# Optimization experiments

Hardware: AMD Instinct MI355X
Metric: run time of the kernel (lower is better)

## Reference

```python
import jax, jax.numpy as jnp
import numpy as np

VOCAB, EMB, HID, FF, NCLS = 1000, 32, 32, 16, 7
T, B = 512, 512


def setup_inputs() -> dict:
    key = jax.random.key(0)
    ks = jax.random.split(key, 10)
    s = 1.0 / np.sqrt(HID)
    return {
        "x": jax.random.randint(ks[0], (T, B), 0, VOCAB, dtype=jnp.int64)
        if jax.config.jax_enable_x64 else jax.random.randint(ks[0], (T, B), 0, VOCAB, dtype=jnp.int32),
        "emb": jax.random.normal(ks[1], (VOCAB, EMB), dtype=jnp.float32),
        "W_ih": jax.random.uniform(ks[2], (4 * HID, EMB), minval=-s, maxval=s, dtype=jnp.float32),
        "W_hh": jax.random.uniform(ks[3], (4 * HID, HID), minval=-s, maxval=s, dtype=jnp.float32),
        "b_ih": jax.random.uniform(ks[4], (4 * HID,), minval=-s, maxval=s, dtype=jnp.float32),
        "b_hh": jax.random.uniform(ks[5], (4 * HID,), minval=-s, maxval=s, dtype=jnp.float32),
        "W1": jax.random.uniform(ks[6], (FF, HID), minval=-s, maxval=s, dtype=jnp.float32),
        "b1": jax.random.uniform(ks[7], (FF,), minval=-s, maxval=s, dtype=jnp.float32),
        "W2": jax.random.uniform(ks[8], (NCLS, FF), minval=-s, maxval=s, dtype=jnp.float32),
        "b2": jax.random.uniform(ks[9], (NCLS,), minval=-s, maxval=s, dtype=jnp.float32),
    }


def _lstm(xg, W_hh):
    # xg: (T, B, 4H) precomputed input-to-gate projections (incl. both biases)
    Bn = xg.shape[1]
    h0 = jnp.zeros((Bn, HID), xg.dtype)
    c0 = jnp.zeros((Bn, HID), xg.dtype)

    def step(carry, xg_t):
        h, c = carry
        g = xg_t + h @ W_hh.T  # (B, 4H)
        i, f, gg, o = jnp.split(g, 4, axis=-1)  # PyTorch gate order i,f,g,o
        i = jax.nn.sigmoid(i)
        f = jax.nn.sigmoid(f)
        gg = jnp.tanh(gg)
        o = jax.nn.sigmoid(o)
        c = f * c + i * gg
        h = o * jnp.tanh(c)
        return (h, c), h

    _, hs = jax.lax.scan(step, (h0, c0), xg)
    return hs  # (T, B, H)


def reference(x, emb, W_ih, W_hh, b_ih, b_hh, W1, b1, W2, b2):
    e = emb[x]  # (T, B, EMB) embedding lookup
    xg = jnp.einsum('tbe,ge->tbg', e, W_ih) + b_ih + b_hh  # (T, B, 4H)
    hs = _lstm(xg, W_hh)  # (T, B, H)
    z = jax.nn.relu(jnp.einsum('tbh,fh->tbf', hs, W1) + b1)  # (T, B, FF)
    logits = jnp.einsum('tbf,cf->tbc', z, W2) + b2  # (T, B, NCLS)
    # torch F.softmax with dim=None on a 3D tensor softmaxes over dim 0
    return jax.nn.softmax(logits, axis=0)
```

## Files before the change

### kernel.cpp

```cpp
#include <hip/hip_runtime.h>
#include <math.h>

#define TT    512
#define BB    512
#define HID   32
#define EMB   32
#define FFD   16
#define NCLS  7
#define VOCABN 1000

typedef float v2f __attribute__((ext_vector_type(2)));
typedef float v4f __attribute__((ext_vector_type(4)));

#define NLOG2E  (-1.4426950408889634f)
#define N2LOG2E (-2.8853900817779268f)

__device__ __forceinline__ float rl(float v, int k) {
    return __int_as_float(__builtin_amdgcn_readlane(__float_as_int(v), k));
}
__device__ __forceinline__ float fast_rcp(float x) {
#if defined(__has_builtin)
#if __has_builtin(__builtin_amdgcn_rcpf)
    return __builtin_amdgcn_rcpf(x);
#else
    return 1.0f / x;
#endif
#else
    return 1.0f / x;
#endif
}
__device__ __forceinline__ float sigf(float x) { return fast_rcp(1.0f + __expf(-x)); }
__device__ __forceinline__ float tanh_fast(float x) { return 2.0f * sigf(2.0f * x) - 1.0f; }

__device__ __forceinline__ v2f fma2(v2f a, v2f b, v2f c) {
#if defined(__has_builtin)
#if __has_builtin(__builtin_elementwise_fma)
    return __builtin_elementwise_fma(a, b, c);
#else
    v2f r; r.x = fmaf(a.x, b.x, c.x); r.y = fmaf(a.y, b.y, c.y); return r;
#endif
#else
    v2f r; r.x = fmaf(a.x, b.x, c.x); r.y = fmaf(a.y, b.y, c.y); return r;
#endif
}

__device__ __forceinline__ float xhalf_swap(float v) {
#if defined(__has_builtin)
#if __has_builtin(__builtin_amdgcn_permlane32_swap)
    const unsigned u = __float_as_uint(v);
    auto r = __builtin_amdgcn_permlane32_swap(u, u, false, false);
    return __uint_as_float((r[0] ^ r[1]) ^ u);
#else
    return __shfl_xor(v, 32);
#endif
#else
    return __shfl_xor(v, 32);
#endif
}

__global__ __launch_bounds__(64) void build_xg(
    const float* __restrict__ emb, const float* __restrict__ W_ih,
    const float* __restrict__ b_ih, const float* __restrict__ b_hh,
    float2* __restrict__ tab, int scaled)
{
    const int v = blockIdx.x;
    const int j = threadIdx.x;
    const float* e  = emb + v * EMB;
    const float* w0 = W_ih + j * EMB;
    const float* w1 = W_ih + (j + 64) * EMB;
    float a0 = b_ih[j]      + b_hh[j];
    float a1 = b_ih[j + 64] + b_hh[j + 64];
    #pragma unroll
    for (int k = 0; k < EMB; ++k) {
        const float ek = e[k];
        a0 = fmaf(w0[k], ek, a0);
        a1 = fmaf(w1[k], ek, a1);
    }
    float s0 = 1.0f, s1 = 1.0f;
    if (scaled) { s0 = NLOG2E; s1 = (j < 32) ? N2LOG2E : NLOG2E; }
    tab[v * 64 + j] = make_float2(a0 * s0, a1 * s1);
}

__global__ __launch_bounds__(64)
__attribute__((amdgpu_waves_per_eu(1, 1)))
void lstm_fused(
    const int* __restrict__ x, const float2* __restrict__ tab,
    const float* __restrict__ W_hh,
    const float* __restrict__ W1, const float* __restrict__ b1,
    const float* __restrict__ W2, const float* __restrict__ b2,
    float* __restrict__ out)
{
    const int b  = blockIdx.x;
    const int j  = threadIdx.x;
    const int m  = j & 31;
    const bool lo = j < 32;

    __shared__ __align__(16) float sh[8 * HID];
    __shared__ __align__(16) float shlg2[TT][17];

    const float fA = NLOG2E;
    const float fB = lo ? N2LOG2E : NLOG2E;
    const v2f sA2 = {fA, fA};
    const v2f sB2 = {fB, fB};
    const v4f* WA = (const v4f*)(W_hh + j * HID);
    const v4f* WB = (const v4f*)(W_hh + (j + 64) * HID);
    v4f t;
    v2f wpa0,wpa1,wpa2,wpa3,wpa4,wpa5,wpa6,wpa7,wpa8,wpa9,wpa10,wpa11,wpa12,wpa13,wpa14,wpa15;
    v2f wpb0,wpb1,wpb2,wpb3,wpb4,wpb5,wpb6,wpb7,wpb8,wpb9,wpb10,wpb11,wpb12,wpb13,wpb14,wpb15;
    t = WA[0]; wpa0  = t.lo * sA2; wpa1  = t.hi * sA2;
    t = WA[1]; wpa2  = t.lo * sA2; wpa3  = t.hi * sA2;
    t = WA[2]; wpa4  = t.lo * sA2; wpa5  = t.hi * sA2;
    t = WA[3]; wpa6  = t.lo * sA2; wpa7  = t.hi * sA2;
    t = WA[4]; wpa8  = t.lo * sA2; wpa9  = t.hi * sA2;
    t = WA[5]; wpa10 = t.lo * sA2; wpa11 = t.hi * sA2;
    t = WA[6]; wpa12 = t.lo * sA2; wpa13 = t.hi * sA2;
    t = WA[7]; wpa14 = t.lo * sA2; wpa15 = t.hi * sA2;
    t = WB[0]; wpb0  = t.lo * sB2; wpb1  = t.hi * sB2;
    t = WB[1]; wpb2  = t.lo * sB2; wpb3  = t.hi * sB2;
    t = WB[2]; wpb4  = t.lo * sB2; wpb5  = t.hi * sB2;
    t = WB[3]; wpb6  = t.lo * sB2; wpb7  = t.hi * sB2;
    t = WB[4]; wpb8  = t.lo * sB2; wpb9  = t.hi * sB2;
    t = WB[5]; wpb10 = t.lo * sB2; wpb11 = t.hi * sB2;
    t = WB[6]; wpb12 = t.lo * sB2; wpb13 = t.hi * sB2;
    t = WB[7]; wpb14 = t.lo * sB2; wpb15 = t.hi * sB2;

    const int f16 = j & 15;
    v2f w1p0,w1p1,w1p2,w1p3,w1p4,w1p5,w1p6,w1p7,w1p8,w1p9,w1p10,w1p11,w1p12,w1p13,w1p14,w1p15;
    {
        const v4f* W1r = (const v4f*)(W1 + f16 * HID);
        v4f q;
        q = W1r[0]; w1p0  = q.lo; w1p1  = q.hi;
        q = W1r[1]; w1p2  = q.lo; w1p3  = q.hi;
        q = W1r[2]; w1p4  = q.lo; w1p5  = q.hi;
        q = W1r[3]; w1p6  = q.lo; w1p7  = q.hi;
        q = W1r[4]; w1p8  = q.lo; w1p9  = q.hi;
        q = W1r[5]; w1p10 = q.lo; w1p11 = q.hi;
        q = W1r[6]; w1p12 = q.lo; w1p13 = q.hi;
        q = W1r[7]; w1p14 = q.lo; w1p15 = q.hi;
    }
    const float b1v = b1[f16];

    float h = 0.f, c = 0.f;

    auto z_store = [&](int t_out, v4f h0, v4f h1, v4f h2, v4f h3,
                                  v4f h4, v4f h5, v4f h6, v4f h7) {
        v2f z0 = {b1v, 0.f}, z1 = {0.f, 0.f};
        z0 = fma2(w1p0,  h0.lo, z0);  z1 = fma2(w1p1,  h0.hi, z1);
        z0 = fma2(w1p2,  h1.lo, z0);  z1 = fma2(w1p3,  h1.hi, z1);
        z0 = fma2(w1p4,  h2.lo, z0);  z1 = fma2(w1p5,  h2.hi, z1);
        z0 = fma2(w1p6,  h3.lo, z0);  z1 = fma2(w1p7,  h3.hi, z1);
        z0 = fma2(w1p8,  h4.lo, z0);  z1 = fma2(w1p9,  h4.hi, z1);
        z0 = fma2(w1p10, h5.lo, z0);  z1 = fma2(w1p11, h5.hi, z1);
        z0 = fma2(w1p12, h6.lo, z0);  z1 = fma2(w1p13, h6.hi, z1);
        z0 = fma2(w1p14, h7.lo, z0);  z1 = fma2(w1p15, h7.hi, z1);
        const v2f zs = z0 + z1;
        const float z = fmaxf(zs.x + zs.y, 0.0f);
        if (j < 16) shlg2[t_out][j] = z;
    };

    if (lo) sh[7 * HID + m] = 0.0f;

    int xiB[8];
    float2 cxg[8];
    {
        int xi0[8];
        #pragma unroll
        for (int u = 0; u < 8; ++u) xi0[u] = x[u * BB + b];
        #pragma unroll
        for (int u = 0; u < 8; ++u) xiB[u] = x[(8 + u) * BB + b];
        #pragma unroll
        for (int u = 0; u < 8; ++u) cxg[u] = tab[(size_t)xi0[u] * 64 + j];
    }

    for (int t8 = 0; t8 < TT / 8; ++t8) {
        float2 nxg[8];
        #pragma unroll
        for (int u = 0; u < 8; ++u) nxg[u] = tab[(size_t)xiB[u] * 64 + j];
        int xiN[8];
        const int nb2 = (t8 + 2 < TT / 8) ? (t8 + 2) * 8 : 0;
        #pragma unroll
        for (int u = 0; u < 8; ++u) xiN[u] = x[(nb2 + u) * BB + b];

        #pragma unroll
        for (int u = 0; u < 8; ++u) {
            const float* hb = sh + ((u + 7) & 7) * HID;
            const v4f h0 = *(const v4f*)(hb + 0);
            const v4f h1 = *(const v4f*)(hb + 4);
            const v4f h2 = *(const v4f*)(hb + 8);
            const v4f h3 = *(const v4f*)(hb + 12);
            const v4f h4 = *(const v4f*)(hb + 16);
            const v4f h5 = *(const v4f*)(hb + 20);
            const v4f h6 = *(const v4f*)(hb + 24);
            const v4f h7 = *(const v4f*)(hb + 28);

            v2f aP0 = {cxg[u].x, 0.f}, aP1 = {0.f, 0.f};
            v2f aQ0 = {cxg[u].y, 0.f}, aQ1 = {0.f, 0.f};
            aP0 = fma2(wpa0,  h0.lo, aP0);  aP1 = fma2(wpa1,  h0.hi, aP1);
            aQ0 = fma2(wpb0,  h0.lo, aQ0);  aQ1 = fma2(wpb1,  h0.hi, aQ1);
            aP0 = fma2(wpa2,  h1.lo, aP0);  aP1 = fma2(wpa3,  h1.hi, aP1);
            aQ0 = fma2(wpb2,  h1.lo, aQ0);  aQ1 = fma2(wpb3,  h1.hi, aQ1);
            aP0 = fma2(wpa4,  h2.lo, aP0);  aP1 = fma2(wpa5,  h2.hi, aP1);
            aQ0 = fma2(wpb4,  h2.lo, aQ0);  aQ1 = fma2(wpb5,  h2.hi, aQ1);
            aP0 = fma2(wpa6,  h3.lo, aP0);  aP1 = fma2(wpa7,  h3.hi, aP1);
            aQ0 = fma2(wpb6,  h3.lo, aQ0);  aQ1 = fma2(wpb7,  h3.hi, aQ1);
            aP0 = fma2(wpa8,  h4.lo, aP0);  aP1 = fma2(wpa9,  h4.hi, aP1);
            aQ0 = fma2(wpb8,  h4.lo, aQ0);  aQ1 = fma2(wpb9,  h4.hi, aQ1);
            aP0 = fma2(wpa10, h5.lo, aP0);  aP1 = fma2(wpa11, h5.hi, aP1);
            aQ0 = fma2(wpb10, h5.lo, aQ0);  aQ1 = fma2(wpb11, h5.hi, aQ1);
            aP0 = fma2(wpa12, h6.lo, aP0);  aP1 = fma2(wpa13, h6.hi, aP1);
            aQ0 = fma2(wpb12, h6.lo, aQ0);  aQ1 = fma2(wpb13, h6.hi, aQ1);
            aP0 = fma2(wpa14, h7.lo, aP0);  aP1 = fma2(wpa15, h7.hi, aP1);
            aQ0 = fma2(wpb14, h7.lo, aQ0);  aQ1 = fma2(wpb15, h7.hi, aQ1);
            const v2f aP = aP0 + aP1;
            const v2f aQ = aQ0 + aQ1;
            const float accA = aP.x + aP.y;
            const float accB = aQ.x + aQ.y;

            const float actA = fast_rcp(1.0f + __builtin_exp2f(accA));
            const float sgB  = fast_rcp(1.0f + __builtin_exp2f(accB));
            const float actB = lo ? fmaf(2.0f, sgB, -1.0f) : sgB;
            const float oA = xhalf_swap(actA);
            const float oB = xhalf_swap(actB);
            const float gi = lo ? actA : oA;
            const float gf = lo ? oA   : actA;
            const float gg = lo ? actB : oB;
            const float go = lo ? oB   : actB;
            c = fmaf(gf, c, gi * gg);
            const float tc = fmaf(2.0f,
                fast_rcp(1.0f + __builtin_exp2f(c * N2LOG2E)), -1.0f);
            h = go * tc;

            if (lo) sh[u * HID + m] = h;

            if (t8 + u > 0)
                z_store(t8 * 8 + u - 1, h0, h1, h2, h3, h4, h5, h6, h7);
        }

        #pragma unroll
        for (int u = 0; u < 8; ++u) { cxg[u] = nxg[u]; xiB[u] = xiN[u]; }
    }

    {
        const float* hb = sh + 7 * HID;
        const v4f h0 = *(const v4f*)(hb + 0);
        const v4f h1 = *(const v4f*)(hb + 4);
        const v4f h2 = *(const v4f*)(hb + 8);
        const v4f h3 = *(const v4f*)(hb + 12);
        const v4f h4 = *(const v4f*)(hb + 16);
        const v4f h5 = *(const v4f*)(hb + 20);
        const v4f h6 = *(const v4f*)(hb + 24);
        const v4f h7 = *(const v4f*)(hb + 28);
        z_store(TT - 1, h0, h1, h2, h3, h4, h5, h6, h7);
    }

    float lg[8][NCLS];
    #pragma unroll
    for (int i = 0; i < 8; ++i) {
        const int tt = j + 64 * i;
        float zz[FFD];
        #pragma unroll
        for (int f = 0; f < FFD; ++f) zz[f] = shlg2[tt][f];
        #pragma unroll
        for (int cc = 0; cc < NCLS; ++cc) {
            float a0 = b2[cc], a1 = 0.f, a2 = 0.f, a3 = 0.f;
            #pragma unroll
            for (int f = 0; f < FFD; f += 4) {
                a0 = fmaf(W2[cc * FFD + f],     zz[f],     a0);
                a1 = fmaf(W2[cc * FFD + f + 1], zz[f + 1], a1);
                a2 = fmaf(W2[cc * FFD + f + 2], zz[f + 2], a2);
                a3 = fmaf(W2[cc * FFD + f + 3], zz[f + 3], a3);
            }
            lg[i][cc] = (a0 + a1) + (a2 + a3);
        }
    }
    #pragma unroll
    for (int cc = 0; cc < NCLS; ++cc) {
        float mm = lg[0][cc];
        #pragma unroll
        for (int i = 1; i < 8; ++i) mm = fmaxf(mm, lg[i][cc]);
        #pragma unroll
        for (int off = 32; off; off >>= 1) mm = fmaxf(mm, __shfl_xor(mm, off));
        float ss = 0.f;
        #pragma unroll
        for (int i = 0; i < 8; ++i) { lg[i][cc] = __expf(lg[i][cc] - mm); ss += lg[i][cc]; }
        #pragma unroll
        for (int off = 32; off; off >>= 1) ss += __shfl_xor(ss, off);
        const float ic = fast_rcp(ss);
        #pragma unroll
        for (int i = 0; i < 8; ++i) lg[i][cc] *= ic;
    }
    #pragma unroll
    for (int i = 0; i < 8; ++i) {
        const int tt = j + 64 * i;
        float* op = out + ((size_t)tt * BB + b) * NCLS;
        #pragma unroll
        for (int cc = 0; cc < NCLS; ++cc) op[cc] = lg[i][cc];
    }
}

template <bool TAB>
__global__ __launch_bounds__(64) void lstm_all(
    const int* __restrict__ x, const float* __restrict__ emb,
    const float* __restrict__ W_ih, const float* __restrict__ W_hh,
    const float* __restrict__ b_ih, const float* __restrict__ b_hh,
    const float* __restrict__ W1, const float* __restrict__ b1,
    const float* __restrict__ W2, const float* __restrict__ b2,
    const float2* __restrict__ tab, float* __restrict__ out)
{
    const int b  = blockIdx.x;
    const int j  = threadIdx.x;
    const int m  = j & 31;
    const bool lo = j < 32;
    const int rA = j, rB = j + 64;

    float whhA[HID], whhB[HID];
    #pragma unroll
    for (int k = 0; k < HID; k += 4) {
        float4 a;
        a = *(const float4*)(W_hh + rA * HID + k); whhA[k]=a.x; whhA[k+1]=a.y; whhA[k+2]=a.z; whhA[k+3]=a.w;
        a = *(const float4*)(W_hh + rB * HID + k); whhB[k]=a.x; whhB[k+1]=a.y; whhB[k+2]=a.z; whhB[k+3]=a.w;
    }
    float wihA[HID], wihB[HID];
    float biasA = 0.f, biasB = 0.f;
    if constexpr (!TAB) {
        #pragma unroll
        for (int k = 0; k < HID; k += 4) {
            float4 a;
            a = *(const float4*)(W_ih + rA * HID + k); wihA[k]=a.x; wihA[k+1]=a.y; wihA[k+2]=a.z; wihA[k+3]=a.w;
            a = *(const float4*)(W_ih + rB * HID + k); wihB[k]=a.x; wihB[k+1]=a.y; wihB[k+2]=a.z; wihB[k+3]=a.w;
        }
        biasA = b_ih[rA] + b_hh[rA];
        biasB = b_ih[rB] + b_hh[rB];
    }
    const int f16 = j & 15;
    float w1r[HID];
    #pragma unroll
    for (int k = 0; k < HID; ++k) w1r[k] = W1[f16 * HID + k];
    const int cls = j & 7;
    const int c7  = (cls < NCLS) ? cls : 0;
    float w2r[FFD];
    #pragma unroll
    for (int f = 0; f < FFD; ++f) w2r[f] = W2[c7 * FFD + f];
    const float b1v = b1[f16];
    const float b2v = b2[c7];

    float h = 0.f, c = 0.f;
    float mrun = -3.0e38f, srun = 0.f;

    auto gates = [&](float accA, float accB) {
        const float actA = sigf(accA);
        const float sB   = lo ? 2.0f * accB : accB;
        const float sgB  = sigf(sB);
        const float actB = lo ? 2.0f * sgB - 1.0f : sgB;
        const float oA = __shfl_xor(actA, 32);
        const float oB = __shfl_xor(actB, 32);
        const float gi = lo ? actA : oA;
        const float gf = lo ? oA   : actA;
        const float gg = lo ? actB : oB;
        const float go = lo ? oB   : actB;
        c = fmaf(gf, c, gi * gg);
        h = go * tanh_fast(c);
    };

    auto ff_head = [&](int t_out, const float* hsv) {
        float z0 = b1v, z1 = 0.f;
        #pragma unroll
        for (int k = 0; k < HID; k += 2) {
            z0 = fmaf(w1r[k],     hsv[k],     z0);
            z1 = fmaf(w1r[k + 1], hsv[k + 1], z1);
        }
        const float z = fmaxf(z0 + z1, 0.0f);
        float lgv = b2v;
        #pragma unroll
        for (int f = 0; f < FFD; ++f) lgv = fmaf(w2r[f], rl(z, f), lgv);
        const float mn = fmaxf(mrun, lgv);
        srun = fmaf(srun, __expf(mrun - mn), __expf(lgv - mn));
        mrun = mn;
        if (j < NCLS) out[(t_out * BB + b) * NCLS + j] = lgv;
    };

    int xvn1 = x[1 * BB + b];
    int xvn2 = x[2 * BB + b];
    float2 xg = make_float2(0.f, 0.f);
    float eA = 0.f;
    if constexpr (TAB) xg = tab[(size_t)x[b] * 64 + j];
    else               eA = emb[x[b] * EMB + m];

    if constexpr (TAB) {
        gates(xg.x, xg.y);
    } else {
        float es[EMB];
        #pragma unroll
        for (int k = 0; k < EMB; ++k) es[k] = rl(eA, k);
        float p0 = biasA, p1 = 0.f, q0 = biasB, q1 = 0.f;
        #pragma unroll
        for (int k = 0; k < EMB; k += 2) {
            p0 = fmaf(wihA[k],   es[k],   p0); p1 = fmaf(wihA[k+1], es[k+1], p1);
            q0 = fmaf(wihB[k],   es[k],   q0); q1 = fmaf(wihB[k+1], es[k+1], q1);
        }
        gates(p0 + p1, q0 + q1);
    }
    if constexpr (TAB) xg = tab[(size_t)xvn1 * 64 + j];
    else               eA = emb[xvn1 * EMB + m];
    xvn1 = xvn2;
    xvn2 = x[3 * BB + b];

    for (int t = 1; t < TT; ++t) {
        float2 xg_n = make_float2(0.f, 0.f);
        float  e_n  = 0.f;
        if (t + 1 < TT) {
            if constexpr (TAB) xg_n = tab[(size_t)xvn1 * 64 + j];
            else               e_n  = emb[xvn1 * EMB + m];
        }
        const int xv_n3 = (t + 3 < TT) ? x[(t + 3) * BB + b] : 0;

        float hsv[HID];
        #pragma unroll
        for (int k = 0; k < HID; ++k) hsv[k] = rl(h, k);

        ff_head(t - 1, hsv);

        float p0, p1 = 0.f, q0, q1 = 0.f;
        if constexpr (TAB) { p0 = xg.x; q0 = xg.y; }
        else               { p0 = biasA; q0 = biasB; }
        if constexpr (!TAB) {
            float es[EMB];
            #pragma unroll
            for (int k = 0; k < EMB; ++k) es[k] = rl(eA, k);
            #pragma unroll
            for (int k = 0; k < EMB; k += 2) {
                p0 = fmaf(wihA[k],   es[k],   p0); p1 = fmaf(wihA[k+1], es[k+1], p1);
                q0 = fmaf(wihB[k],   es[k],   q0); q1 = fmaf(wihB[k+1], es[k+1], q1);
            }
        }
        #pragma unroll
        for (int k = 0; k < HID; k += 2) {
            p0 = fmaf(whhA[k],   hsv[k],   p0); p1 = fmaf(whhA[k+1], hsv[k+1], p1);
            q0 = fmaf(whhB[k],   hsv[k],   q0); q1 = fmaf(whhB[k+1], hsv[k+1], q1);
        }
        gates(p0 + p1, q0 + q1);

        xg = xg_n; eA = e_n; xvn1 = xvn2; xvn2 = xv_n3;
    }

    {
        float hsv[HID];
        #pragma unroll
        for (int k = 0; k < HID; ++k) hsv[k] = rl(h, k);
        ff_head(TT - 1, hsv);
    }

    #pragma unroll 1
    for (int cc = 0; cc < NCLS; ++cc) {
        const float mc = rl(mrun, cc);
        const float sc = rl(srun, cc);
        const float ic = 1.0f / sc;
        #pragma unroll
        for (int i = 0; i < TT / 64; ++i) {
            const int t = j + 64 * i;
            const int a = (t * BB + b) * NCLS + cc;
            out[a] = __expf(out[a] - mc) * ic;
        }
    }
}

extern "C" void kernel_launch(void* const* d_in, const int* in_sizes, int n_in,
                              void* d_out, int out_size, void* d_ws, size_t ws_size,
                              hipStream_t stream) {
    const int*   x   = (const int*)  d_in[0];
    const float* emb = (const float*)d_in[1];
    const float* Wih = (const float*)d_in[2];
    const float* Whh = (const float*)d_in[3];
    const float* bih = (const float*)d_in[4];
    const float* bhh = (const float*)d_in[5];
    const float* W1  = (const float*)d_in[6];
    const float* b1  = (const float*)d_in[7];
    const float* W2  = (const float*)d_in[8];
    const float* b2  = (const float*)d_in[9];
    float* out = (float*)d_out;

    const size_t tab_bytes = (size_t)VOCABN * 128 * sizeof(float);
    if (ws_size >= tab_bytes) {
        float2* tab = (float2*)d_ws;
        build_xg<<<VOCABN, 64, 0, stream>>>(emb, Wih, bih, bhh, tab, 1);
        lstm_fused<<<BB, 64, 0, stream>>>(x, tab, Whh, W1, b1, W2, b2, out);
    } else {
        lstm_all<false><<<BB, 64, 0, stream>>>(x, emb, Wih, Whh, bih, bhh,
                                               W1, b1, W2, b2, nullptr, out);
    }
}
```

Measured before the change: 253.2 us.

## Defer W1 projection until after recurrence by storing full hidden history in LDS

Removes the per-timestep W1 projection and ReLU from the serial recurrence loop. Every hidden state is now kept in a 64KB shared buffer, and z is computed after the scan with each thread handling 8 timesteps. This shortens the latency-bound critical path of the recurrence. In exchange it adds LDS footprint, uniform W1 loads from global/scalar memory, and a post-loop phase with more work per thread.

```diff
diff --git a/kernel.cpp b/kernel.cpp
--- a/kernel.cpp
+++ b/kernel.cpp
@@ -95,8 +95,7 @@
     const int m  = j & 31;
     const bool lo = j < 32;
 
-    __shared__ __align__(16) float sh[8 * HID];
-    __shared__ __align__(16) float shlg2[TT][17];
+    __shared__ __align__(16) float sh_h[TT * HID];
 
     const float fA = NLOG2E;
     const float fB = lo ? N2LOG2E : NLOG2E;
@@ -124,41 +123,9 @@
     t = WB[6]; wpb12 = t.lo * sB2; wpb13 = t.hi * sB2;
     t = WB[7]; wpb14 = t.lo * sB2; wpb15 = t.hi * sB2;
 
-    const int f16 = j & 15;
-    v2f w1p0,w1p1,w1p2,w1p3,w1p4,w1p5,w1p6,w1p7,w1p8,w1p9,w1p10,w1p11,w1p12,w1p13,w1p14,w1p15;
-    {
-        const v4f* W1r = (const v4f*)(W1 + f16 * HID);
-        v4f q;
-        q = W1r[0]; w1p0  = q.lo; w1p1  = q.hi;
-        q = W1r[1]; w1p2  = q.lo; w1p3  = q.hi;
-        q = W1r[2]; w1p4  = q.lo; w1p5  = q.hi;
-        q = W1r[3]; w1p6  = q.lo; w1p7  = q.hi;
-        q = W1r[4]; w1p8  = q.lo; w1p9  = q.hi;
-        q = W1r[5]; w1p10 = q.lo; w1p11 = q.hi;
-        q = W1r[6]; w1p12 = q.lo; w1p13 = q.hi;
-        q = W1r[7]; w1p14 = q.lo; w1p15 = q.hi;
-    }
-    const float b1v = b1[f16];
-
     float h = 0.f, c = 0.f;
 
-    auto z_store = [&](int t_out, v4f h0, v4f h1, v4f h2, v4f h3,
-                                  v4f h4, v4f h5, v4f h6, v4f h7) {
-        v2f z0 = {b1v, 0.f}, z1 = {0.f, 0.f};
-        z0 = fma2(w1p0,  h0.lo, z0);  z1 = fma2(w1p1,  h0.hi, z1);
-        z0 = fma2(w1p2,  h1.lo, z0);  z1 = fma2(w1p3,  h1.hi, z1);
-        z0 = fma2(w1p4,  h2.lo, z0);  z1 = fma2(w1p5,  h2.hi, z1);
-        z0 = fma2(w1p6,  h3.lo, z0);  z1 = fma2(w1p7,  h3.hi, z1);
-        z0 = fma2(w1p8,  h4.lo, z0);  z1 = fma2(w1p9,  h4.hi, z1);
-        z0 = fma2(w1p10, h5.lo, z0);  z1 = fma2(w1p11, h5.hi, z1);
-        z0 = fma2(w1p12, h6.lo, z0);  z1 = fma2(w1p13, h6.hi, z1);
-        z0 = fma2(w1p14, h7.lo, z0);  z1 = fma2(w1p15, h7.hi, z1);
-        const v2f zs = z0 + z1;
-        const float z = fmaxf(zs.x + zs.y, 0.0f);
-        if (j < 16) shlg2[t_out][j] = z;
-    };
-
-    if (lo) sh[7 * HID + m] = 0.0f;
+    if (lo) sh_h[(TT - 1) * HID + m] = 0.0f;
 
     int xiB[8];
     float2 cxg[8];
@@ -183,7 +150,8 @@
 
         #pragma unroll
         for (int u = 0; u < 8; ++u) {
-            const float* hb = sh + ((u + 7) & 7) * HID;
+            const int rp = (t8 * 8 + u + TT - 1) & (TT - 1);
+            const float* hb = sh_h + rp * HID;
             const v4f h0 = *(const v4f*)(hb + 0);
             const v4f h1 = *(const v4f*)(hb + 4);
             const v4f h2 = *(const v4f*)(hb + 8);
@@ -230,36 +198,37 @@
                 fast_rcp(1.0f + __builtin_exp2f(c * N2LOG2E)), -1.0f);
             h = go * tc;
 
-            if (lo) sh[u * HID + m] = h;
-
-            if (t8 + u > 0)
-                z_store(t8 * 8 + u - 1, h0, h1, h2, h3, h4, h5, h6, h7);
+            if (lo) sh_h[(t8 * 8 + u) * HID + m] = h;
         }
 
         #pragma unroll
         for (int u = 0; u < 8; ++u) { cxg[u] = nxg[u]; xiB[u] = xiN[u]; }
-    }
-
-    {
-        const float* hb = sh + 7 * HID;
-        const v4f h0 = *(const v4f*)(hb + 0);
-        const v4f h1 = *(const v4f*)(hb + 4);
-        const v4f h2 = *(const v4f*)(hb + 8);
-        const v4f h3 = *(const v4f*)(hb + 12);
-        const v4f h4 = *(const v4f*)(hb + 16);
-        const v4f h5 = *(const v4f*)(hb + 20);
-        const v4f h6 = *(const v4f*)(hb + 24);
-        const v4f h7 = *(const v4f*)(hb + 28);
-        z_store(TT - 1, h0, h1, h2, h3, h4, h5, h6, h7);
     }
 
     float lg[8][NCLS];
     #pragma unroll
     for (int i = 0; i < 8; ++i) {
         const int tt = j + 64 * i;
+        const float* hr = sh_h + tt * HID;
+        float hv[32];
+        #pragma unroll
+        for (int k = 0; k < HID; k += 4) {
+            const v4f q = *(const v4f*)(hr + k);
+            hv[k] = q.x; hv[k + 1] = q.y; hv[k + 2] = q.z; hv[k + 3] = q.w;
+        }
         float zz[FFD];
         #pragma unroll
-        for (int f = 0; f < FFD; ++f) zz[f] = shlg2[tt][f];
+        for (int f = 0; f < FFD; ++f) {
+            float a0 = b1[f], a1 = 0.f, a2 = 0.f, a3 = 0.f;
+            #pragma unroll
+            for (int k = 0; k < HID; k += 4) {
+                a0 = fmaf(W1[f * HID + k],     hv[k],     a0);
+                a1 = fmaf(W1[f * HID + k + 1], hv[k + 1], a1);
+                a2 = fmaf(W1[f * HID + k + 2], hv[k + 2], a2);
+                a3 = fmaf(W1[f * HID + k + 3], hv[k + 3], a3);
+            }
+            zz[f] = fmaxf((a0 + a1) + (a2 + a3), 0.f);
+        }
         #pragma unroll
         for (int cc = 0; cc < NCLS; ++cc) {
             float a0 = b2[cc], a1 = 0.f, a2 = 0.f, a3 = 0.f;
```

Result: no change. 254.7 us (+0.6%).
